# Optimization experiments

Hardware: AMD Instinct MI355X
Metric: run time of the kernel (lower is better)

## Reference

```python
import jax, jax.numpy as jnp
import numpy as np

B, N, E = 2, 16000, 160000
NDIMS, NMEAS, NMODES = 2, 1, 128
IN_DIM, OUT_DIM, FC_DIM = 3, 1, 128
LAYERS = [64, 64, 64, 64]
INV_MIN, INV_MAX = 0.5, 2.0


def setup_inputs() -> dict:
    key = jax.random.key(0)
    ks = jax.random.split(key, 16)
    L = len(LAYERS) - 1
    C = LAYERS[0]
    scale = 1.0 / (C * C)
    u = lambda k, sh, s: jax.random.uniform(k, sh, jnp.float32, -s, s)
    inp = {}
    inp["x"] = jax.random.normal(ks[0], (B, N, IN_DIM), jnp.float32)
    inp["node_mask"] = jnp.ones((B, N, 1), jnp.int32)
    inp["nodes"] = jax.random.uniform(ks[1], (B, N, NDIMS), jnp.float32)
    inp["node_weights"] = jax.random.uniform(ks[2], (B, N, NMEAS), jnp.float32) / N
    inp["directed_edges"] = jax.random.randint(ks[3], (B, E, 2), 0, N, jnp.int32)
    inp["edge_gradient_weights"] = jax.random.normal(ks[4], (B, E, NDIMS), jnp.float32)
    inp["modes"] = jax.random.normal(ks[5], (NMODES, NDIMS, NMEAS), jnp.float32)
    # scaled_logit(1.0, 0.5, 2.0) = log(0.5/1.0)
    inp["inv_L_scale_latent"] = jnp.full((NDIMS, NMEAS), np.log((1.0 - INV_MIN) / (INV_MAX - 1.0)), jnp.float32)
    inp["fc0_W"] = u(ks[6], (C, IN_DIM), 1.0 / np.sqrt(IN_DIM))
    inp["fc0_b"] = jnp.zeros((C,), jnp.float32)
    inp["weights_c"] = u(ks[7], (L, C, C, NMODES, NMEAS), scale)
    inp["weights_s"] = u(ks[8], (L, C, C, NMODES, NMEAS), scale)
    inp["weights_0"] = u(ks[9], (L, C, C, 1, NMEAS), scale)
    inp["ws_W"] = u(ks[10], (L, C, C), 1.0 / np.sqrt(C))
    inp["ws_b"] = jnp.zeros((L, C), jnp.float32)
    inp["gws_W"] = u(ks[11], (L, C, C * NDIMS), 1.0 / np.sqrt(C * NDIMS))
    inp["gws_b"] = jnp.zeros((L, C), jnp.float32)
    inp["fc1_W"] = u(ks[12], (FC_DIM, C), 1.0 / np.sqrt(C))
    inp["fc1_b"] = jnp.zeros((FC_DIM,), jnp.float32)
    inp["fc2_W"] = u(ks[13], (OUT_DIM, FC_DIM), 1.0 / np.sqrt(FC_DIM))
    inp["fc2_b"] = jnp.zeros((OUT_DIM,), jnp.float32)
    return inp


def _forward(x, nodes, node_weights, edge_gradient_weights, modes, inv_L_scale_latent,
             fc0_W, fc0_b, weights_c, weights_s, weights_0, ws_W, ws_b, gws_W, gws_b,
             fc1_W, fc1_b, fc2_W, fc2_b, directed_edges):
    L = weights_c.shape[0]
    n = x.shape[1]
    # scaled sigmoid of latent inverse length scale
    inv_L = INV_MIN + (INV_MAX - INV_MIN) * jax.nn.sigmoid(inv_L_scale_latent)
    smodes = modes * inv_L  # [K, D, W]
    # Fourier bases over all nodes
    temp = jnp.einsum('bxd,kdw->bxkw', nodes, smodes)  # [B, N, K, W]
    bases_c, bases_s = jnp.cos(temp), jnp.sin(temp)
    bases_0 = jnp.ones(temp.shape[:2] + (1, temp.shape[-1]), temp.dtype)
    wnw = node_weights[:, :, None, :]  # [B, N, 1, W]
    wbases_c, wbases_s, wbases_0 = bases_c * wnw, bases_s * wnw, bases_0 * wnw

    tgt = directed_edges[..., 0]  # [B, E]
    src = directed_edges[..., 1]

    def grad_field(f):  # f: [B, C, N] -> [B, C*D, N]
        ft = jnp.transpose(f, (0, 2, 1))  # [B, N, C]
        f_src = jnp.take_along_axis(ft, src[..., None], axis=1)  # [B, E, C]
        f_tgt = jnp.take_along_axis(ft, tgt[..., None], axis=1)
        diff = f_src - f_tgt
        msg = jnp.einsum('bed,bec->becd', edge_gradient_weights, diff)  # [B, E, C, D]
        msg = msg.reshape(msg.shape[0], msg.shape[1], -1)  # [B, E, C*D]
        seg = jax.vmap(lambda m, t: jax.ops.segment_sum(m, t, num_segments=n))(msg, tgt)
        return jnp.transpose(seg, (0, 2, 1))  # [B, C*D, N]

    # lift: fc0 acts on channel dim
    h = jnp.einsum('oi,bni->bon', fc0_W, x) + fc0_b[None, :, None]  # [B, C, N]

    for i in range(L):
        # spectral conv with explicit bases
        x_c = jnp.einsum('bix,bxkw->bikw', h, wbases_c)
        x_s = -jnp.einsum('bix,bxkw->bikw', h, wbases_s)
        x_0 = jnp.einsum('bix,bxkw->bikw', h, wbases_0)
        f_c = jnp.einsum('bikw,iokw->bokw', x_c, weights_c[i]) - jnp.einsum('bikw,iokw->bokw', x_s, weights_s[i])
        f_s = jnp.einsum('bikw,iokw->bokw', x_s, weights_c[i]) + jnp.einsum('bikw,iokw->bokw', x_c, weights_s[i])
        f_0 = jnp.einsum('bikw,iokw->bokw', x_0, weights_0[i])
        x1 = (jnp.einsum('bokw,bxkw->box', f_0, bases_0)
              + 2 * jnp.einsum('bokw,bxkw->box', f_c, bases_c)
              - 2 * jnp.einsum('bokw,bxkw->box', f_s, bases_s))
        # pointwise linear W
        x2 = jnp.einsum('oi,bin->bon', ws_W[i], h) + ws_b[i][None, :, None]
        # differential operator D: gradient then linear
        x3 = jnp.einsum('oi,bin->bon', gws_W[i], grad_field(h)) + gws_b[i][None, :, None]
        h = x1 + x2 + x3
        if i < L - 1:
            h = jax.nn.gelu(h)

    out = jnp.transpose(h, (0, 2, 1))  # [B, N, C]
    out = jax.nn.gelu(jnp.einsum('oc,bnc->bno', fc1_W, out) + fc1_b)
    out = jnp.einsum('oc,bnc->bno', fc2_W, out) + fc2_b
    return out  # [B, N, out_dim]


def reference(x, node_mask, nodes, node_weights, directed_edges, edge_gradient_weights,
              modes, inv_L_scale_latent, fc0_W, fc0_b, weights_c, weights_s, weights_0,
              ws_W, ws_b, gws_W, gws_b, fc1_W, fc1_b, fc2_W, fc2_b):
    del node_mask  # padding mask; all-ones here, not used in the core math
    return _forward(x, nodes, node_weights, edge_gradient_weights, modes, inv_L_scale_latent,
                    fc0_W, fc0_b, weights_c, weights_s, weights_0, ws_W, ws_b, gws_W, gws_b,
                    fc1_W, fc1_b, fc2_W, fc2_b, directed_edges)
```

## Files before the change

### kernel.cpp

```cpp
#include <hip/hip_runtime.h>
#include <math.h>

#define BB 2
#define NN 16000
#define EE 160000
#define KK 128
#define CC 64
#define LL 3
#define RDIM 448
#define S1 125
#define XR 128

__device__ __forceinline__ float gelu_f(float x){
    float x3 = x * x * x;
    return 0.5f * x * (1.f + tanhf(0.7978845608028654f * (x + 0.044715f * x3)));
}

__device__ __forceinline__ void gl2lds16(const float* g, float* l){
    __builtin_amdgcn_global_load_lds(
        (const __attribute__((address_space(1))) void*)g,
        (__attribute__((address_space(3))) void*)l, 16, 0, 0);
}

__global__ __launch_bounds__(256) void k_bases(
    const float* __restrict__ nodes, const float* __restrict__ modes,
    const float* __restrict__ latent, float* __restrict__ cb, float* __restrict__ sb){
    int bid = blockIdx.x;
    int b = bid / 500, x0 = (bid % 500) * 32;
    int t = threadIdx.x;
    __shared__ float sm0[128], sm1[128];
    if (t < 128){
        float i0 = 0.5f + 1.5f / (1.f + expf(-latent[0]));
        float i1 = 0.5f + 1.5f / (1.f + expf(-latent[1]));
        sm0[t] = modes[t*2+0] * i0;
        sm1[t] = modes[t*2+1] * i1;
    }
    __syncthreads();
    int k = t & 127, xh = t >> 7;
    for (int p = 0; p < 16; p++){
        int x = x0 + p*2 + xh;
        size_t nb = (size_t)b*NN + x;
        float n0 = nodes[nb*2], n1 = nodes[nb*2+1];
        float tmp = n0*sm0[k] + n1*sm1[k];
        float sv, cv; sincosf(tmp, &sv, &cv);
        cb[nb*KK + k] = cv;
        sb[nb*KK + k] = sv;
    }
}

__global__ __launch_bounds__(256) void k_fc0(
    const float* __restrict__ x, const float* __restrict__ W,
    const float* __restrict__ bb, float* __restrict__ h0){
    int bid = blockIdx.x;
    int b = bid / 250, x0 = (bid % 250) * 64;
    int t = threadIdx.x, o = t & 63, xg = t >> 6;
    float w0 = W[o*3], w1 = W[o*3+1], w2 = W[o*3+2], bo = bb[o];
    for (int xi = xg; xi < 64; xi += 4){
        size_t xb = (size_t)b*NN + x0 + xi;
        float v0 = x[xb*3], v1 = x[xb*3+1], v2 = x[xb*3+2];
        h0[xb*CC + o] = w0*v0 + w1*v1 + w2*v2 + bo;
    }
}

__global__ __launch_bounds__(256) void csr_hist(
    const int* __restrict__ edges, int* __restrict__ cnt){
    int idx = blockIdx.x * 256 + threadIdx.x;
    if (idx >= BB*EE) return;
    int b = idx / EE;
    int tgt = edges[(size_t)idx*2];
    atomicAdd(&cnt[b*NN + tgt], 1);
}

__global__ __launch_bounds__(1024) void csr_scan(
    const int* __restrict__ cnt, int* __restrict__ rowptr, int* __restrict__ cursor){
    int b = blockIdx.x;
    int t = threadIdx.x;
    __shared__ int lds[1024];
    int base = t * 16;
    int v[16];
    int run = 0;
    #pragma unroll
    for (int j = 0; j < 16; j++){
        int n = base + j;
        int c = (n < NN) ? cnt[b*NN + n] : 0;
        v[j] = run;
        run += c;
    }
    lds[t] = run;
    __syncthreads();
    for (int off = 1; off < 1024; off <<= 1){
        int xv = (t >= off) ? lds[t-off] : 0;
        __syncthreads();
        lds[t] += xv;
        __syncthreads();
    }
    int toff = lds[t] - run;
    #pragma unroll
    for (int j = 0; j < 16; j++){
        int n = base + j;
        if (n < NN){
            int p = toff + v[j];
            rowptr[b*(NN+1) + n] = p;
            cursor[b*NN + n] = p;
        }
    }
    if (t == 1023) rowptr[b*(NN+1) + NN] = lds[1023];
}

__global__ __launch_bounds__(256) void csr_fill(
    const int* __restrict__ edges, const float* __restrict__ egw,
    int* __restrict__ cursor, int* __restrict__ insrc, float2* __restrict__ inw){
    int idx = blockIdx.x * 256 + threadIdx.x;
    if (idx >= BB*EE) return;
    int b = idx / EE;
    int tgt = edges[(size_t)idx*2];
    int src = edges[(size_t)idx*2 + 1];
    int pos = atomicAdd(&cursor[b*NN + tgt], 1);
    insrc[(size_t)b*EE + pos] = src;
    const float2 wv = *(const float2*)&egw[(size_t)idx*2];
    inw[(size_t)b*EE + pos] = wv;
}

struct FwdBuf {
    float hT[16*64];
    float wcT[16*128];
    float wsT[16*128];
    float wv[16];
};

__global__ __launch_bounds__(256) void k1_fwd(
    const float* __restrict__ h, const float* __restrict__ cb,
    const float* __restrict__ sb, const float* __restrict__ nw,
    float* __restrict__ partC, float* __restrict__ partS, float* __restrict__ part0){
    int bid = blockIdx.x;
    int b = bid / S1, s = bid % S1;
    int t = threadIdx.x;
    __shared__ __align__(16) FwdBuf bufs[2];
    int kg = t & 15, ig = t >> 4;
    float accC[4][8] = {};
    float accS[4][8] = {};
    float acc0[4] = {};
    int xbase = s * XR;

    auto STAGE = [&](FwdBuf* d, int ch){
        int xs = xbase + ch*16;
        const float* hb  = &h [((size_t)b*NN + xs)*CC];
        const float* cbb = &cb[((size_t)b*NN + xs)*KK];
        const float* sbb = &sb[((size_t)b*NN + xs)*KK];
        gl2lds16(hb + t*4, &d->hT[(t>>6)*256]);
        #pragma unroll
        for (int rep = 0; rep < 2; rep++){
            int u = rep*256 + t;
            gl2lds16(cbb + u*4, &d->wcT[(u>>6)*256]);
            gl2lds16(sbb + u*4, &d->wsT[(u>>6)*256]);
        }
        if (t < 16) d->wv[t] = nw[b*NN + xs + t];
    };

    STAGE(&bufs[0], 0);
    int cur = 0;
    for (int ch = 0; ch < XR/16; ch++){
        __syncthreads();
        if (ch < XR/16 - 1) STAGE(&bufs[cur^1], ch+1);
        FwdBuf* d = &bufs[cur];
        #pragma unroll
        for (int xx = 0; xx < 16; xx++){
            float wgt = d->wv[xx];
            float4 hv = *(float4*)&d->hT[xx*64 + ig*4];
            float ha0 = hv.x*wgt, ha1 = hv.y*wgt, ha2 = hv.z*wgt, ha3 = hv.w*wgt;
            acc0[0] += ha0; acc0[1] += ha1; acc0[2] += ha2; acc0[3] += ha3;
            #pragma unroll
            for (int j = 0; j < 8; j++){
                int kq = kg + 16*j;
                float cv = d->wcT[xx*128 + kq];
                float sv = d->wsT[xx*128 + kq];
                accC[0][j] += ha0*cv; accC[1][j] += ha1*cv;
                accC[2][j] += ha2*cv; accC[3][j] += ha3*cv;
                accS[0][j] += ha0*sv; accS[1][j] += ha1*sv;
                accS[2][j] += ha2*sv; accS[3][j] += ha3*sv;
            }
        }
        cur ^= 1;
    }
    size_t pbase = (size_t)(b*S1 + s) * CC;
    #pragma unroll
    for (int ii = 0; ii < 4; ii++){
        int i = ig*4 + ii;
        #pragma unroll
        for (int j = 0; j < 8; j++){
            int k = kg + 16*j;
            partC[(pbase + i)*KK + k] = accC[ii][j];
            partS[(pbase + i)*KK + k] = accS[ii][j];
        }
        if (kg == 0) part0[pbase + i] = acc0[ii];
    }
}

__global__ __launch_bounds__(256) void k1_reduce(
    const float* __restrict__ partC, const float* __restrict__ partS,
    float* __restrict__ Sc, float* __restrict__ Ss){
    int b = blockIdx.x >> 6, i = blockIdx.x & 63;
    int t = threadIdx.x;
    int k = t & 127, sh = t >> 7;
    float c0=0,c1=0,c2=0,c3=0, q0=0,q1=0,q2=0,q3=0;
    int s = sh;
    for (; s + 6 < S1; s += 8){
        size_t i0 = ((size_t)(b*S1 + s    )*CC + i)*KK + k;
        size_t i1 = ((size_t)(b*S1 + s + 2)*CC + i)*KK + k;
        size_t i2 = ((size_t)(b*S1 + s + 4)*CC + i)*KK + k;
        size_t i3 = ((size_t)(b*S1 + s + 6)*CC + i)*KK + k;
        c0 += partC[i0]; c1 += partC[i1]; c2 += partC[i2]; c3 += partC[i3];
        q0 += partS[i0]; q1 += partS[i1]; q2 += partS[i2]; q3 += partS[i3];
    }
    for (; s < S1; s += 2){
        size_t i0 = ((size_t)(b*S1 + s)*CC + i)*KK + k;
        c0 += partC[i0]; q0 += partS[i0];
    }
    float sc = (c0+c1)+(c2+c3), ss = (q0+q1)+(q2+q3);
    __shared__ float rC[128], rS[128];
    if (sh){ rC[k] = sc; rS[k] = ss; }
    __syncthreads();
    if (!sh){
        Sc[((size_t)b*CC + i)*KK + k] = sc + rC[k];
        Ss[((size_t)b*CC + i)*KK + k] = ss + rS[k];
    }
}

__global__ __launch_bounds__(256) void k2_mix(
    const float* __restrict__ Sc, const float* __restrict__ Ss,
    const float* __restrict__ part0,
    const float* __restrict__ wc, const float* __restrict__ wsp,
    const float* __restrict__ w0,
    const float* __restrict__ wsb, const float* __restrict__ gwsb,
    const float* __restrict__ wsW, const float* __restrict__ gwsW,
    float* __restrict__ Wbig, float* __restrict__ bias, int l){
    int b = blockIdx.x >> 6, o = blockIdx.x & 63;
    int t = threadIdx.x;
    __shared__ float fc2s[2][128], fs2s[2][128];
    __shared__ float red[64];
    if (t < 64){
        float x0 = 0.f;
        for (int s = 0; s < S1; s++) x0 += part0[(b*S1+s)*CC + t];
        red[t] = x0 * w0[((size_t)l*CC + t)*CC + o];
    }
    int k = t & 127, hf = t >> 7;
    float fc = 0.f, fs = 0.f;
    for (int i = hf*32; i < hf*32 + 32; i++){
        float sc = Sc[(b*CC + i)*KK + k];
        float ss = Ss[(b*CC + i)*KK + k];
        size_t wi = (((size_t)l*CC + i)*CC + o)*KK + k;
        float a = wc[wi], bb2 = wsp[wi];
        fc += sc*a + ss*bb2;
        fs += sc*bb2 - ss*a;
    }
    fc2s[hf][k] = fc; fs2s[hf][k] = fs;
    __syncthreads();
    size_t wb = ((size_t)b*CC + o) * RDIM;
    if (t < 128){
        float FC = fc2s[0][t] + fc2s[1][t];
        float FS = fs2s[0][t] + fs2s[1][t];
        Wbig[wb + t] = 2.f * FC;
        Wbig[wb + 128 + t] = -2.f * FS;
    }
    if (t < 64) Wbig[wb + 256 + t] = wsW[((size_t)l*CC + o)*CC + t];
    if (t >= 64 && t < 192) Wbig[wb + 320 + (t-64)] = gwsW[((size_t)l*CC + o)*128 + (t-64)];
    if (t == 0){
        float f0 = 0.f;
        for (int i = 0; i < 64; i++) f0 += red[i];
        bias[b*CC + o] = f0 + wsb[l*CC + o] + gwsb[l*CC + o];
    }
}

__global__ __launch_bounds__(256) void k_grad(
    const float* __restrict__ h, const int* __restrict__ rowptr,
    const int* __restrict__ insrc, const float2* __restrict__ inw,
    float* __restrict__ seg){
    int bid = blockIdx.x;
    int b = bid / 1000, n0 = (bid % 1000) * 16;
    int w = threadIdx.x >> 6, c = threadIdx.x & 63;
    const float*  hb  = h + (size_t)b*NN*CC;
    const int*    isb = insrc + (size_t)b*EE;
    const float2* iwb = inw + (size_t)b*EE;
    #pragma unroll
    for (int g = 0; g < 4; g++){
        int n = n0 + w*4 + g;
        float hn = hb[(size_t)n*CC + c];
        int p0 = rowptr[b*(NN+1) + n];
        int p1 = rowptr[b*(NN+1) + n + 1];
        float a0 = 0.f, a1 = 0.f;
        int p = p0;
        for (; p + 4 <= p1; p += 4){
            int s0 = isb[p], s1 = isb[p+1], s2 = isb[p+2], s3 = isb[p+3];
            float2 w0 = iwb[p], w1 = iwb[p+1], w2 = iwb[p+2], w3 = iwb[p+3];
            float d0 = hb[(size_t)s0*CC + c] - hn;
            float d1 = hb[(size_t)s1*CC + c] - hn;
            float d2 = hb[(size_t)s2*CC + c] - hn;
            float d3 = hb[(size_t)s3*CC + c] - hn;
            a0 += w0.x*d0 + w1.x*d1 + w2.x*d2 + w3.x*d3;
            a1 += w0.y*d0 + w1.y*d1 + w2.y*d2 + w3.y*d3;
        }
        for (; p < p1; p++){
            int sx = isb[p]; float2 ww = iwb[p];
            float d = hb[(size_t)sx*CC + c] - hn;
            a0 += ww.x*d; a1 += ww.y*d;
        }
        *(float2*)&seg[((size_t)b*NN + n)*128 + 2*c] = make_float2(a0, a1);
    }
}

__global__ __launch_bounds__(256) void k3_gemm(
    const float* __restrict__ Wbig, const float* __restrict__ bias,
    const float* __restrict__ cbase, const float* __restrict__ sbase,
    const float* __restrict__ h, const float* __restrict__ seg,
    float* __restrict__ hout, int applyGelu){
    int bid = blockIdx.x;
    int b = bid / 250, x0 = (bid % 250) * 64;
    int t = threadIdx.x;
    __shared__ __align__(16) float Wl[32][68];
    __shared__ __align__(16) float Vl[32][68];
    int to = t & 15, tx = t >> 4;
    int o0 = to*4, xl = tx*4;
    float acc[4][4] = {};
    for (int ch = 0; ch < 14; ch++){
        const float* src; int kb, rl;
        if (ch < 4){ src = cbase; kb = ch*32; rl = 128; }
        else if (ch < 8){ src = sbase; kb = (ch-4)*32; rl = 128; }
        else if (ch < 10){ src = h; kb = (ch-8)*32; rl = 64; }
        else { src = seg; kb = (ch-10)*32; rl = 128; }
        #pragma unroll
        for (int rep = 0; rep < 2; rep++){
            int u = rep*256 + t;
            int xx = u >> 3, kq = u & 7;
            float4 v = *(const float4*)&src[((size_t)b*NN + x0 + xx)*rl + kb + kq*4];
            Vl[kq*4+0][xx] = v.x; Vl[kq*4+1][xx] = v.y;
            Vl[kq*4+2][xx] = v.z; Vl[kq*4+3][xx] = v.w;
        }
        #pragma unroll
        for (int rep = 0; rep < 2; rep++){
            int u = rep*256 + t;
            int oo = u >> 3, kq = u & 7;
            float4 v = *(const float4*)&Wbig[((size_t)b*CC + oo)*RDIM + ch*32 + kq*4];
            Wl[kq*4+0][oo] = v.x; Wl[kq*4+1][oo] = v.y;
            Wl[kq*4+2][oo] = v.z; Wl[kq*4+3][oo] = v.w;
        }
        __syncthreads();
        #pragma unroll
        for (int kk = 0; kk < 32; kk++){
            float4 wvec = *(float4*)&Wl[kk][o0];
            float4 vvec = *(float4*)&Vl[kk][xl];
            float wa[4] = {wvec.x, wvec.y, wvec.z, wvec.w};
            float va[4] = {vvec.x, vvec.y, vvec.z, vvec.w};
            #pragma unroll
            for (int j = 0; j < 4; j++)
                #pragma unroll
                for (int i = 0; i < 4; i++)
                    acc[j][i] += va[j] * wa[i];
        }
        __syncthreads();
    }
    float bs[4];
    #pragma unroll
    for (int i = 0; i < 4; i++) bs[i] = bias[b*CC + o0 + i];
    #pragma unroll
    for (int j = 0; j < 4; j++){
        float4 r;
        r.x = acc[j][0] + bs[0];
        r.y = acc[j][1] + bs[1];
        r.z = acc[j][2] + bs[2];
        r.w = acc[j][3] + bs[3];
        if (applyGelu){
            r.x = gelu_f(r.x); r.y = gelu_f(r.y);
            r.z = gelu_f(r.z); r.w = gelu_f(r.w);
        }
        *(float4*)&hout[((size_t)b*NN + x0 + xl + j)*CC + o0] = r;
    }
}

__global__ __launch_bounds__(256) void k_head(
    const float* __restrict__ h, const float* __restrict__ W1,
    const float* __restrict__ b1, const float* __restrict__ W2,
    const float* __restrict__ b2, float* __restrict__ out){
    int bid = blockIdx.x;
    int b = bid / 250, n0 = (bid % 250) * 64;
    int t = threadIdx.x, w = t >> 6, f = t & 63;
    __shared__ float Wl[128][65];
    #pragma unroll
    for (int r = 0; r < 8; r++){
        int u = r*256 + t;
        int ff = u >> 4, cq = u & 15;
        float4 v = *(const float4*)&W1[ff*64 + cq*4];
        Wl[ff][cq*4+0] = v.x; Wl[ff][cq*4+1] = v.y;
        Wl[ff][cq*4+2] = v.z; Wl[ff][cq*4+3] = v.w;
    }
    __syncthreads();
    float w2a = W2[f], w2b = W2[64+f];
    float b1a = b1[f], b1b = b1[64+f];
    float b2v = b2[0];
    for (int g = 0; g < 16; g++){
        int n = n0 + w*16 + g;
        float hv = h[((size_t)b*NN + n)*CC + f];
        float a1 = b1a, a2 = b1b;
        #pragma unroll
        for (int c2 = 0; c2 < 64; c2++){
            float xv = __shfl(hv, c2, 64);
            a1 += Wl[f][c2] * xv;
            a2 += Wl[64+f][c2] * xv;
        }
        float p = gelu_f(a1)*w2a + gelu_f(a2)*w2b;
        for (int off = 32; off; off >>= 1) p += __shfl_down(p, off, 64);
        if (f == 0) out[(size_t)b*NN + n] = p + b2v;
    }
}

extern "C" void kernel_launch(void* const* d_in, const int* in_sizes, int n_in,
                              void* d_out, int out_size, void* d_ws, size_t ws_size,
                              hipStream_t stream){
    const float* x_in  = (const float*)d_in[0];
    const float* nodes = (const float*)d_in[2];
    const float* nw    = (const float*)d_in[3];
    const int*   edges = (const int*)d_in[4];
    const float* egw   = (const float*)d_in[5];
    const float* modes = (const float*)d_in[6];
    const float* latent= (const float*)d_in[7];
    const float* fc0W  = (const float*)d_in[8];
    const float* fc0b  = (const float*)d_in[9];
    const float* wc    = (const float*)d_in[10];
    const float* wsp   = (const float*)d_in[11];
    const float* w0    = (const float*)d_in[12];
    const float* wsW   = (const float*)d_in[13];
    const float* wsb   = (const float*)d_in[14];
    const float* gwsW  = (const float*)d_in[15];
    const float* gwsb  = (const float*)d_in[16];
    const float* fc1W  = (const float*)d_in[17];
    const float* fc1b  = (const float*)d_in[18];
    const float* fc2W  = (const float*)d_in[19];
    const float* fc2b  = (const float*)d_in[20];
    float* out = (float*)d_out;

    char* wsbase = (char*)d_ws;
    size_t off = 0;
    auto alloc = [&](size_t bytes) -> void* {
        void* p = wsbase + off;
        off += (bytes + 255) & ~(size_t)255;
        return p;
    };
    float* cb    = (float*)alloc((size_t)BB*NN*KK*4);
    float* sb    = (float*)alloc((size_t)BB*NN*KK*4);
    float* h0    = (float*)alloc((size_t)BB*NN*CC*4);
    float* h1    = (float*)alloc((size_t)BB*NN*CC*4);
    float* seg   = (float*)alloc((size_t)BB*NN*2*CC*4);
    float* partC = (float*)alloc((size_t)BB*S1*CC*KK*4);
    float* partS = (float*)alloc((size_t)BB*S1*CC*KK*4);
    float* part0 = (float*)alloc((size_t)BB*S1*CC*4);
    float* Sc    = (float*)alloc((size_t)BB*CC*KK*4);
    float* Ss    = (float*)alloc((size_t)BB*CC*KK*4);
    float* Wbig  = (float*)alloc((size_t)BB*CC*RDIM*4);
    float* bias  = (float*)alloc((size_t)BB*CC*4);
    int*   cnt   = (int*)alloc((size_t)BB*NN*4);
    int*   rowptr= (int*)alloc((size_t)BB*(NN+4)*4);
    int*   cursor= (int*)alloc((size_t)BB*NN*4);
    int*   insrc = (int*)alloc((size_t)BB*EE*4);
    float2* inw  = (float2*)alloc((size_t)BB*EE*8);

    k_bases<<<BB*500, 256, 0, stream>>>(nodes, modes, latent, cb, sb);
    k_fc0<<<BB*250, 256, 0, stream>>>(x_in, fc0W, fc0b, h0);

    hipMemsetAsync(cnt, 0, (size_t)BB*NN*4, stream);
    csr_hist<<<(BB*EE+255)/256, 256, 0, stream>>>(edges, cnt);
    csr_scan<<<BB, 1024, 0, stream>>>(cnt, rowptr, cursor);
    csr_fill<<<(BB*EE+255)/256, 256, 0, stream>>>(edges, egw, cursor, insrc, inw);

    float* hcur = h0;
    float* hnext = h1;
    for (int l = 0; l < LL; l++){
        k1_fwd<<<BB*S1, 256, 0, stream>>>(hcur, cb, sb, nw, partC, partS, part0);
        k1_reduce<<<BB*CC, 256, 0, stream>>>(partC, partS, Sc, Ss);
        k2_mix<<<BB*CC, 256, 0, stream>>>(Sc, Ss, part0, wc, wsp, w0, wsb, gwsb,
                                          wsW, gwsW, Wbig, bias, l);
        k_grad<<<BB*1000, 256, 0, stream>>>(hcur, rowptr, insrc, inw, seg);
        k3_gemm<<<BB*250, 256, 0, stream>>>(Wbig, bias, cb, sb, hcur, seg, hnext,
                                            (l < LL-1) ? 1 : 0);
        float* tmp = hcur; hcur = hnext; hnext = tmp;
    }
    k_head<<<BB*250, 256, 0, stream>>>(hcur, fc1W, fc1b, fc2W, fc2b, out);
    (void)in_sizes; (void)n_in; (void)out_size; (void)ws_size;
}
```

Measured before the change: 521.4 us.

## Port spectral and mixing GEMMs to split-bf16 MFMA with precomputed transposed operands

Replaces the FP32 FMA loops in k1_fwd and k3_gemm with bf16 MFMA 16x16x32 instructions. Each FP32 operand is split into high and low bf16 parts and three products are accumulated to stay close to FP32 accuracy. The bases kernel, fc0 and the GEMM epilogue now also emit transposed, node-weighted hi/lo copies, and fc0 and k3 produce part0 directly, with reduce and grad kernels reshaped to match. The aim is to trade scalar FMA throughput for matrix-core throughput, at the cost of extra memory traffic for the duplicated bf16 buffers and a small precision risk.

```diff
diff --git a/kernel.cpp b/kernel.cpp
--- a/kernel.cpp
+++ b/kernel.cpp
@@ -7,59 +7,208 @@
 #define KK 128
 #define CC 64
 #define LL 3
-#define RDIM 448
-#define S1 125
-#define XR 128
+
+typedef __attribute__((ext_vector_type(8))) short bf16x8;
+typedef __attribute__((ext_vector_type(4))) float f32x4;
 
 __device__ __forceinline__ float gelu_f(float x){
     float x3 = x * x * x;
     return 0.5f * x * (1.f + tanhf(0.7978845608028654f * (x + 0.044715f * x3)));
 }
-
-__device__ __forceinline__ void gl2lds16(const float* g, float* l){
-    __builtin_amdgcn_global_load_lds(
-        (const __attribute__((address_space(1))) void*)g,
-        (__attribute__((address_space(3))) void*)l, 16, 0, 0);
-}
+__device__ __forceinline__ ushort f2bf(float f){
+    uint u = __float_as_uint(f);
+    u += 0x7fff + ((u >> 16) & 1);
+    return (ushort)(u >> 16);
+}
+__device__ __forceinline__ float bf2f(ushort h){ return __uint_as_float(((uint)h) << 16); }
+__device__ __forceinline__ void fsplit(float v, ushort &hi, ushort &lo){
+    hi = f2bf(v);
+    lo = f2bf(v - bf2f(hi));
+}
+__device__ __forceinline__ uint pk2(ushort a, ushort b){ return (uint)a | ((uint)b << 16); }
 
 __global__ __launch_bounds__(256) void k_bases(
     const float* __restrict__ nodes, const float* __restrict__ modes,
-    const float* __restrict__ latent, float* __restrict__ cb, float* __restrict__ sb){
+    const float* __restrict__ latent, const float* __restrict__ nw,
+    ushort* __restrict__ cbh, ushort* __restrict__ cbl,
+    ushort* __restrict__ sbh, ushort* __restrict__ sbl,
+    ushort* __restrict__ wTh, ushort* __restrict__ wTl){
     int bid = blockIdx.x;
-    int b = bid / 500, x0 = (bid % 500) * 32;
+    int b = bid / 250, x0 = (bid % 250) * 64;
     int t = threadIdx.x;
-    __shared__ float sm0[128], sm1[128];
+    __shared__ float sm0[128], sm1[128], nwv[64];
+    __shared__ uint tc[64][65], ts[64][65];
     if (t < 128){
         float i0 = 0.5f + 1.5f / (1.f + expf(-latent[0]));
         float i1 = 0.5f + 1.5f / (1.f + expf(-latent[1]));
         sm0[t] = modes[t*2+0] * i0;
         sm1[t] = modes[t*2+1] * i1;
     }
-    __syncthreads();
-    int k = t & 127, xh = t >> 7;
-    for (int p = 0; p < 16; p++){
-        int x = x0 + p*2 + xh;
-        size_t nb = (size_t)b*NN + x;
-        float n0 = nodes[nb*2], n1 = nodes[nb*2+1];
-        float tmp = n0*sm0[k] + n1*sm1[k];
-        float sv, cv; sincosf(tmp, &sv, &cv);
-        cb[nb*KK + k] = cv;
-        sb[nb*KK + k] = sv;
+    if (t < 64) nwv[t] = nw[b*NN + x0 + t];
+    __syncthreads();
+    int xloc = t & 63;
+    float n0 = nodes[((size_t)b*NN + x0 + xloc)*2 + 0];
+    float n1 = nodes[((size_t)b*NN + x0 + xloc)*2 + 1];
+    for (int kh = 0; kh < 2; kh++){
+        int kq = t >> 6;
+        #pragma unroll
+        for (int j = 0; j < 16; j++){
+            int kl = kq*16 + j;
+            int k = kh*64 + kl;
+            float tmp = n0*sm0[k] + n1*sm1[k];
+            float sv, cv; sincosf(tmp, &sv, &cv);
+            ushort h_, l_;
+            fsplit(cv, h_, l_); tc[xloc][kl] = pk2(h_, l_);
+            fsplit(sv, h_, l_); ts[xloc][kl] = pk2(h_, l_);
+        }
+        __syncthreads();
+        {
+            int q = t >> 6;
+            size_t base = ((size_t)b*NN + x0 + xloc)*128 + kh*64 + q*16;
+            #pragma unroll
+            for (int g2 = 0; g2 < 2; g2++){
+                uint u0 = tc[xloc][q*16 + g2*8 + 0], u1 = tc[xloc][q*16 + g2*8 + 1];
+                uint u2 = tc[xloc][q*16 + g2*8 + 2], u3 = tc[xloc][q*16 + g2*8 + 3];
+                uint u4 = tc[xloc][q*16 + g2*8 + 4], u5 = tc[xloc][q*16 + g2*8 + 5];
+                uint u6 = tc[xloc][q*16 + g2*8 + 6], u7 = tc[xloc][q*16 + g2*8 + 7];
+                uint4 vh, vl;
+                vh.x = pk2((ushort)u0,(ushort)u1); vh.y = pk2((ushort)u2,(ushort)u3);
+                vh.z = pk2((ushort)u4,(ushort)u5); vh.w = pk2((ushort)u6,(ushort)u7);
+                vl.x = pk2((ushort)(u0>>16),(ushort)(u1>>16)); vl.y = pk2((ushort)(u2>>16),(ushort)(u3>>16));
+                vl.z = pk2((ushort)(u4>>16),(ushort)(u5>>16)); vl.w = pk2((ushort)(u6>>16),(ushort)(u7>>16));
+                *(uint4*)&cbh[base + g2*8] = vh;
+                *(uint4*)&cbl[base + g2*8] = vl;
+                u0 = ts[xloc][q*16 + g2*8 + 0]; u1 = ts[xloc][q*16 + g2*8 + 1];
+                u2 = ts[xloc][q*16 + g2*8 + 2]; u3 = ts[xloc][q*16 + g2*8 + 3];
+                u4 = ts[xloc][q*16 + g2*8 + 4]; u5 = ts[xloc][q*16 + g2*8 + 5];
+                u6 = ts[xloc][q*16 + g2*8 + 6]; u7 = ts[xloc][q*16 + g2*8 + 7];
+                vh.x = pk2((ushort)u0,(ushort)u1); vh.y = pk2((ushort)u2,(ushort)u3);
+                vh.z = pk2((ushort)u4,(ushort)u5); vh.w = pk2((ushort)u6,(ushort)u7);
+                vl.x = pk2((ushort)(u0>>16),(ushort)(u1>>16)); vl.y = pk2((ushort)(u2>>16),(ushort)(u3>>16));
+                vl.z = pk2((ushort)(u4>>16),(ushort)(u5>>16)); vl.w = pk2((ushort)(u6>>16),(ushort)(u7>>16));
+                *(uint4*)&sbh[base + g2*8] = vh;
+                *(uint4*)&sbl[base + g2*8] = vl;
+            }
+        }
+        {
+            int k = t & 63, g = t >> 6;
+            int kgc = kh*64 + k;
+            int kgs = 128 + kh*64 + k;
+            ushort hc[16], lc[16], hs[16], ls[16];
+            #pragma unroll
+            for (int j = 0; j < 16; j++){
+                int xx = g*16 + j;
+                float wgt = nwv[xx];
+                uint uc = tc[xx][k], us = ts[xx][k];
+                float vc = (bf2f((ushort)uc) + bf2f((ushort)(uc>>16))) * wgt;
+                float vs = (bf2f((ushort)us) + bf2f((ushort)(us>>16))) * wgt;
+                fsplit(vc, hc[j], lc[j]);
+                fsplit(vs, hs[j], ls[j]);
+            }
+            size_t wbc = ((size_t)b*256 + kgc)*16000 + x0 + g*16;
+            size_t wbs = ((size_t)b*256 + kgs)*16000 + x0 + g*16;
+            uint4 v;
+            v.x = pk2(hc[0],hc[1]); v.y = pk2(hc[2],hc[3]); v.z = pk2(hc[4],hc[5]); v.w = pk2(hc[6],hc[7]);
+            *(uint4*)&wTh[wbc] = v;
+            v.x = pk2(hc[8],hc[9]); v.y = pk2(hc[10],hc[11]); v.z = pk2(hc[12],hc[13]); v.w = pk2(hc[14],hc[15]);
+            *(uint4*)&wTh[wbc + 8] = v;
+            v.x = pk2(lc[0],lc[1]); v.y = pk2(lc[2],lc[3]); v.z = pk2(lc[4],lc[5]); v.w = pk2(lc[6],lc[7]);
+            *(uint4*)&wTl[wbc] = v;
+            v.x = pk2(lc[8],lc[9]); v.y = pk2(lc[10],lc[11]); v.z = pk2(lc[12],lc[13]); v.w = pk2(lc[14],lc[15]);
+            *(uint4*)&wTl[wbc + 8] = v;
+            v.x = pk2(hs[0],hs[1]); v.y = pk2(hs[2],hs[3]); v.z = pk2(hs[4],hs[5]); v.w = pk2(hs[6],hs[7]);
+            *(uint4*)&wTh[wbs] = v;
+            v.x = pk2(hs[8],hs[9]); v.y = pk2(hs[10],hs[11]); v.z = pk2(hs[12],hs[13]); v.w = pk2(hs[14],hs[15]);
+            *(uint4*)&wTh[wbs + 8] = v;
+            v.x = pk2(ls[0],ls[1]); v.y = pk2(ls[2],ls[3]); v.z = pk2(ls[4],ls[5]); v.w = pk2(ls[6],ls[7]);
+            *(uint4*)&wTl[wbs] = v;
+            v.x = pk2(ls[8],ls[9]); v.y = pk2(ls[10],ls[11]); v.z = pk2(ls[12],ls[13]); v.w = pk2(ls[14],ls[15]);
+            *(uint4*)&wTl[wbs + 8] = v;
+        }
+        __syncthreads();
+    }
+}
+
+__device__ __forceinline__ void write_h_outputs(
+    const float* ot, const float* nws, int b, int s, int x0, int t, int doAux,
+    float* __restrict__ hx, ushort* __restrict__ hxh, ushort* __restrict__ hxl,
+    ushort* __restrict__ hwh, ushort* __restrict__ hwl, float* __restrict__ part0){
+    {
+        int xl = t >> 1, half = t & 1;
+        size_t gb = ((size_t)b*NN + x0 + xl)*64 + half*32;
+        const float* row = &ot[xl*68 + half*32];
+        #pragma unroll
+        for (int j = 0; j < 8; j++){
+            float4 v; v.x = row[j*4]; v.y = row[j*4+1]; v.z = row[j*4+2]; v.w = row[j*4+3];
+            *(float4*)&hx[gb + j*4] = v;
+        }
+        if (doAux){
+            #pragma unroll
+            for (int q = 0; q < 4; q++){
+                ushort h_[8], l_[8];
+                #pragma unroll
+                for (int j = 0; j < 8; j++) fsplit(row[q*8 + j], h_[j], l_[j]);
+                uint4 vh, vl;
+                vh.x = pk2(h_[0],h_[1]); vh.y = pk2(h_[2],h_[3]); vh.z = pk2(h_[4],h_[5]); vh.w = pk2(h_[6],h_[7]);
+                vl.x = pk2(l_[0],l_[1]); vl.y = pk2(l_[2],l_[3]); vl.z = pk2(l_[4],l_[5]); vl.w = pk2(l_[6],l_[7]);
+                *(uint4*)&hxh[gb + q*8] = vh;
+                *(uint4*)&hxl[gb + q*8] = vl;
+            }
+        }
+    }
+    if (doAux){
+        int i = t & 63, g = t >> 6;
+        float a = 0.f;
+        #pragma unroll
+        for (int rep = 0; rep < 4; rep++){
+            int xs = g*32 + rep*8;
+            ushort h_[8], l_[8];
+            #pragma unroll
+            for (int j = 0; j < 8; j++){
+                float v = ot[(xs + j)*68 + i] * nws[xs + j];
+                a += v;
+                fsplit(v, h_[j], l_[j]);
+            }
+            uint4 vh, vl;
+            vh.x = pk2(h_[0],h_[1]); vh.y = pk2(h_[2],h_[3]); vh.z = pk2(h_[4],h_[5]); vh.w = pk2(h_[6],h_[7]);
+            vl.x = pk2(l_[0],l_[1]); vl.y = pk2(l_[2],l_[3]); vl.z = pk2(l_[4],l_[5]); vl.w = pk2(l_[6],l_[7]);
+            size_t wb = (size_t)(b*64 + i)*16000 + x0 + xs;
+            *(uint4*)&hwh[wb] = vh;
+            *(uint4*)&hwl[wb] = vl;
+        }
+        part0[((size_t)(b*125 + s)*4 + g)*64 + i] = a;
     }
 }
 
 __global__ __launch_bounds__(256) void k_fc0(
     const float* __restrict__ x, const float* __restrict__ W,
-    const float* __restrict__ bb, float* __restrict__ h0){
+    const float* __restrict__ bb, const float* __restrict__ nw,
+    float* __restrict__ hx, ushort* __restrict__ hxh, ushort* __restrict__ hxl,
+    ushort* __restrict__ hwh, ushort* __restrict__ hwl, float* __restrict__ part0){
     int bid = blockIdx.x;
-    int b = bid / 250, x0 = (bid % 250) * 64;
-    int t = threadIdx.x, o = t & 63, xg = t >> 6;
-    float w0 = W[o*3], w1 = W[o*3+1], w2 = W[o*3+2], bo = bb[o];
-    for (int xi = xg; xi < 64; xi += 4){
-        size_t xb = (size_t)b*NN + x0 + xi;
-        float v0 = x[xb*3], v1 = x[xb*3+1], v2 = x[xb*3+2];
-        h0[xb*CC + o] = w0*v0 + w1*v1 + w2*v2 + bo;
-    }
+    int b = bid / 125, s = bid % 125;
+    int x0 = s * 128;
+    int t = threadIdx.x;
+    __shared__ float ot[128*68];
+    __shared__ float nws[128];
+    __shared__ float Wf[192], bf_[64];
+    if (t < 192) Wf[t] = W[t];
+    if (t < 64) bf_[t] = bb[t];
+    if (t < 128) nws[t] = nw[b*NN + x0 + t];
+    __syncthreads();
+    {
+        int xl = t >> 1, half = t & 1;
+        float v0 = x[((size_t)b*NN + x0 + xl)*3 + 0];
+        float v1 = x[((size_t)b*NN + x0 + xl)*3 + 1];
+        float v2 = x[((size_t)b*NN + x0 + xl)*3 + 2];
+        #pragma unroll
+        for (int j = 0; j < 32; j++){
+            int o = half*32 + j;
+            ot[xl*68 + o] = Wf[o*3]*v0 + Wf[o*3+1]*v1 + Wf[o*3+2]*v2 + bf_[o];
+        }
+    }
+    __syncthreads();
+    write_h_outputs(ot, nws, b, s, x0, t, 1, hx, hxh, hxl, hwh, hwl, part0);
 }
 
 __global__ __launch_bounds__(256) void csr_hist(
@@ -121,108 +270,87 @@
     inw[(size_t)b*EE + pos] = wv;
 }
 
-struct FwdBuf {
-    float hT[16*64];
-    float wcT[16*128];
-    float wsT[16*128];
-    float wv[16];
-};
-
 __global__ __launch_bounds__(256) void k1_fwd(
-    const float* __restrict__ h, const float* __restrict__ cb,
-    const float* __restrict__ sb, const float* __restrict__ nw,
-    float* __restrict__ partC, float* __restrict__ partS, float* __restrict__ part0){
+    const ushort* __restrict__ hwH, const ushort* __restrict__ hwL,
+    const ushort* __restrict__ wTH, const ushort* __restrict__ wTL,
+    float* __restrict__ part){
     int bid = blockIdx.x;
-    int b = bid / S1, s = bid % S1;
-    int t = threadIdx.x;
-    __shared__ __align__(16) FwdBuf bufs[2];
-    int kg = t & 15, ig = t >> 4;
-    float accC[4][8] = {};
-    float accS[4][8] = {};
-    float acc0[4] = {};
-    int xbase = s * XR;
-
-    auto STAGE = [&](FwdBuf* d, int ch){
-        int xs = xbase + ch*16;
-        const float* hb  = &h [((size_t)b*NN + xs)*CC];
-        const float* cbb = &cb[((size_t)b*NN + xs)*KK];
-        const float* sbb = &sb[((size_t)b*NN + xs)*KK];
-        gl2lds16(hb + t*4, &d->hT[(t>>6)*256]);
-        #pragma unroll
-        for (int rep = 0; rep < 2; rep++){
-            int u = rep*256 + t;
-            gl2lds16(cbb + u*4, &d->wcT[(u>>6)*256]);
-            gl2lds16(sbb + u*4, &d->wsT[(u>>6)*256]);
-        }
-        if (t < 16) d->wv[t] = nw[b*NN + xs + t];
-    };
-
-    STAGE(&bufs[0], 0);
-    int cur = 0;
-    for (int ch = 0; ch < XR/16; ch++){
-        __syncthreads();
-        if (ch < XR/16 - 1) STAGE(&bufs[cur^1], ch+1);
-        FwdBuf* d = &bufs[cur];
-        #pragma unroll
-        for (int xx = 0; xx < 16; xx++){
-            float wgt = d->wv[xx];
-            float4 hv = *(float4*)&d->hT[xx*64 + ig*4];
-            float ha0 = hv.x*wgt, ha1 = hv.y*wgt, ha2 = hv.z*wgt, ha3 = hv.w*wgt;
-            acc0[0] += ha0; acc0[1] += ha1; acc0[2] += ha2; acc0[3] += ha3;
+    int b = bid / 250, s = bid % 250;
+    int x0 = s * 64;
+    int t = threadIdx.x, l = t & 63, w = t >> 6;
+    __shared__ __align__(16) ushort Bh[128*64], Bl[128*64];
+    f32x4 acc[16] = {};
+    bf16x8 Ah[2], Al[2];
+    int i = w*16 + (l & 15);
+    #pragma unroll
+    for (int ks = 0; ks < 2; ks++){
+        size_t ab = (size_t)(b*64 + i)*16000 + x0 + ks*32 + ((l >> 4) * 8);
+        Ah[ks] = *reinterpret_cast<const bf16x8*>(&hwH[ab]);
+        Al[ks] = *reinterpret_cast<const bf16x8*>(&hwL[ab]);
+    }
+    for (int p = 0; p < 2; p++){
+        #pragma unroll
+        for (int it = 0; it < 4; it++){
+            int u = it*256 + t;
+            int kloc = u >> 3, q = u & 7;
+            size_t g = ((size_t)(b*256 + p*128 + kloc))*16000 + x0 + q*8;
+            uint4 vh = *(const uint4*)&wTH[g];
+            uint4 vl = *(const uint4*)&wTL[g];
+            int ldsb = kloc*128 + ((q*16) ^ ((kloc & 7) << 4));
+            *(uint4*)&Bh[ldsb >> 1] = vh;
+            *(uint4*)&Bl[ldsb >> 1] = vl;
+        }
+        __syncthreads();
+        #pragma unroll
+        for (int kt = 0; kt < 8; kt++){
+            int kcol = kt*16 + (l & 15);
+            int ai = p*8 + kt;
             #pragma unroll
-            for (int j = 0; j < 8; j++){
-                int kq = kg + 16*j;
-                float cv = d->wcT[xx*128 + kq];
-                float sv = d->wsT[xx*128 + kq];
-                accC[0][j] += ha0*cv; accC[1][j] += ha1*cv;
-                accC[2][j] += ha2*cv; accC[3][j] += ha3*cv;
-                accS[0][j] += ha0*sv; accS[1][j] += ha1*sv;
-                accS[2][j] += ha2*sv; accS[3][j] += ha3*sv;
+            for (int ks = 0; ks < 2; ks++){
+                int boff = kcol*128 + (((ks*64) + ((l >> 4) * 16)) ^ ((kcol & 7) << 4));
+                bf16x8 bh = *reinterpret_cast<const bf16x8*>(&Bh[boff >> 1]);
+                bf16x8 bl = *reinterpret_cast<const bf16x8*>(&Bl[boff >> 1]);
+                acc[ai] = __builtin_amdgcn_mfma_f32_16x16x32_bf16(Ah[ks], bh, acc[ai], 0, 0, 0);
+                acc[ai] = __builtin_amdgcn_mfma_f32_16x16x32_bf16(Ah[ks], bl, acc[ai], 0, 0, 0);
+                acc[ai] = __builtin_amdgcn_mfma_f32_16x16x32_bf16(Al[ks], bh, acc[ai], 0, 0, 0);
             }
         }
-        cur ^= 1;
-    }
-    size_t pbase = (size_t)(b*S1 + s) * CC;
-    #pragma unroll
-    for (int ii = 0; ii < 4; ii++){
-        int i = ig*4 + ii;
-        #pragma unroll
-        for (int j = 0; j < 8; j++){
-            int k = kg + 16*j;
-            partC[(pbase + i)*KK + k] = accC[ii][j];
-            partS[(pbase + i)*KK + k] = accS[ii][j];
-        }
-        if (kg == 0) part0[pbase + i] = acc0[ii];
-    }
-}
-
-__global__ __launch_bounds__(256) void k1_reduce(
-    const float* __restrict__ partC, const float* __restrict__ partS,
-    float* __restrict__ Sc, float* __restrict__ Ss){
+        __syncthreads();
+    }
+    size_t pb = (size_t)(b*250 + s) * 64 * 256;
+    #pragma unroll
+    for (int nt = 0; nt < 16; nt++){
+        #pragma unroll
+        for (int r = 0; r < 4; r++){
+            int irow = w*16 + (l >> 4)*4 + r;
+            part[pb + (size_t)irow*256 + nt*16 + (l & 15)] = acc[nt][r];
+        }
+    }
+}
+
+__global__ __launch_bounds__(512) void k1_reduce(
+    const float* __restrict__ part, float* __restrict__ Sc, float* __restrict__ Ss){
     int b = blockIdx.x >> 6, i = blockIdx.x & 63;
     int t = threadIdx.x;
-    int k = t & 127, sh = t >> 7;
-    float c0=0,c1=0,c2=0,c3=0, q0=0,q1=0,q2=0,q3=0;
-    int s = sh;
-    for (; s + 6 < S1; s += 8){
-        size_t i0 = ((size_t)(b*S1 + s    )*CC + i)*KK + k;
-        size_t i1 = ((size_t)(b*S1 + s + 2)*CC + i)*KK + k;
-        size_t i2 = ((size_t)(b*S1 + s + 4)*CC + i)*KK + k;
-        size_t i3 = ((size_t)(b*S1 + s + 6)*CC + i)*KK + k;
-        c0 += partC[i0]; c1 += partC[i1]; c2 += partC[i2]; c3 += partC[i3];
-        q0 += partS[i0]; q1 += partS[i1]; q2 += partS[i2]; q3 += partS[i3];
-    }
-    for (; s < S1; s += 2){
-        size_t i0 = ((size_t)(b*S1 + s)*CC + i)*KK + k;
-        c0 += partC[i0]; q0 += partS[i0];
-    }
-    float sc = (c0+c1)+(c2+c3), ss = (q0+q1)+(q2+q3);
-    __shared__ float rC[128], rS[128];
-    if (sh){ rC[k] = sc; rS[k] = ss; }
+    int c = t & 255, sh = t >> 8;
+    float a0=0,a1=0,a2=0,a3=0;
+    int j = sh;
+    for (; j + 6 < 250; j += 8){
+        a0 += part[((size_t)(b*250 + j    )*64 + i)*256 + c];
+        a1 += part[((size_t)(b*250 + j + 2)*64 + i)*256 + c];
+        a2 += part[((size_t)(b*250 + j + 4)*64 + i)*256 + c];
+        a3 += part[((size_t)(b*250 + j + 6)*64 + i)*256 + c];
+    }
+    for (; j < 250; j += 2)
+        a0 += part[((size_t)(b*250 + j)*64 + i)*256 + c];
+    float sum = (a0+a1)+(a2+a3);
+    __shared__ float r2[256];
+    if (sh) r2[c] = sum;
     __syncthreads();
     if (!sh){
-        Sc[((size_t)b*CC + i)*KK + k] = sc + rC[k];
-        Ss[((size_t)b*CC + i)*KK + k] = ss + rS[k];
+        sum += r2[c];
+        if (c < 128) Sc[(size_t)(b*64 + i)*128 + c] = sum;
+        else         Ss[(size_t)(b*64 + i)*128 + (c - 128)] = sum;
     }
 }
 
@@ -233,21 +361,22 @@
     const float* __restrict__ w0,
     const float* __restrict__ wsb, const float* __restrict__ gwsb,
     const float* __restrict__ wsW, const float* __restrict__ gwsW,
-    float* __restrict__ Wbig, float* __restrict__ bias, int l){
+    ushort* __restrict__ WbH, ushort* __restrict__ WbL,
+    float* __restrict__ bias, int l){
     int b = blockIdx.x >> 6, o = blockIdx.x & 63;
     int t = threadIdx.x;
     __shared__ float fc2s[2][128], fs2s[2][128];
     __shared__ float red[64];
     if (t < 64){
         float x0 = 0.f;
-        for (int s = 0; s < S1; s++) x0 += part0[(b*S1+s)*CC + t];
+        for (int s2 = 0; s2 < 500; s2++) x0 += part0[(size_t)(b*500 + s2)*64 + t];
         red[t] = x0 * w0[((size_t)l*CC + t)*CC + o];
     }
     int k = t & 127, hf = t >> 7;
     float fc = 0.f, fs = 0.f;
     for (int i = hf*32; i < hf*32 + 32; i++){
-        float sc = Sc[(b*CC + i)*KK + k];
-        float ss = Ss[(b*CC + i)*KK + k];
+        float sc = Sc[(size_t)(b*CC + i)*KK + k];
+        float ss = Ss[(size_t)(b*CC + i)*KK + k];
         size_t wi = (((size_t)l*CC + i)*CC + o)*KK + k;
         float a = wc[wi], bb2 = wsp[wi];
         fc += sc*a + ss*bb2;
@@ -255,15 +384,22 @@
     }
     fc2s[hf][k] = fc; fs2s[hf][k] = fs;
     __syncthreads();
-    size_t wb = ((size_t)b*CC + o) * RDIM;
+    size_t wb = (size_t)(b*CC + o) * 448;
     if (t < 128){
         float FC = fc2s[0][t] + fc2s[1][t];
         float FS = fs2s[0][t] + fs2s[1][t];
-        Wbig[wb + t] = 2.f * FC;
-        Wbig[wb + 128 + t] = -2.f * FS;
-    }
-    if (t < 64) Wbig[wb + 256 + t] = wsW[((size_t)l*CC + o)*CC + t];
-    if (t >= 64 && t < 192) Wbig[wb + 320 + (t-64)] = gwsW[((size_t)l*CC + o)*128 + (t-64)];
+        ushort h_, l_;
+        fsplit(2.f*FC, h_, l_);
+        WbH[wb + t] = h_; WbL[wb + t] = l_;
+        fsplit(-2.f*FS, h_, l_);
+        WbH[wb + 128 + t] = h_; WbL[wb + 128 + t] = l_;
+    }
+    if (t < 192){
+        float v = (t < 64) ? wsW[((size_t)l*CC + o)*CC + t]
+                           : gwsW[((size_t)l*CC + o)*128 + (t - 64)];
+        ushort h_, l_; fsplit(v, h_, l_);
+        WbH[wb + 256 + t] = h_; WbL[wb + 256 + t] = l_;
+    }
     if (t == 0){
         float f0 = 0.f;
         for (int i = 0; i < 64; i++) f0 += red[i];
@@ -274,16 +410,16 @@
 __global__ __launch_bounds__(256) void k_grad(
     const float* __restrict__ h, const int* __restrict__ rowptr,
     const int* __restrict__ insrc, const float2* __restrict__ inw,
-    float* __restrict__ seg){
+    ushort* __restrict__ segh, ushort* __restrict__ segl){
     int bid = blockIdx.x;
-    int b = bid / 1000, n0 = (bid % 1000) * 16;
+    int b = bid / 2000, n0 = (bid % 2000) * 8;
     int w = threadIdx.x >> 6, c = threadIdx.x & 63;
     const float*  hb  = h + (size_t)b*NN*CC;
     const int*    isb = insrc + (size_t)b*EE;
     const float2* iwb = inw + (size_t)b*EE;
     #pragma unroll
-    for (int g = 0; g < 4; g++){
-        int n = n0 + w*4 + g;
+    for (int g = 0; g < 2; g++){
+        int n = n0 + w*2 + g;
         float hn = hb[(size_t)n*CC + c];
         int p0 = rowptr[b*(NN+1) + n];
         int p1 = rowptr[b*(NN+1) + n + 1];
@@ -304,76 +440,98 @@
             float d = hb[(size_t)sx*CC + c] - hn;
             a0 += ww.x*d; a1 += ww.y*d;
         }
-        *(float2*)&seg[((size_t)b*NN + n)*128 + 2*c] = make_float2(a0, a1);
+        ushort h0_, l0_, h1_, l1_;
+        fsplit(a0, h0_, l0_);
+        fsplit(a1, h1_, l1_);
+        size_t sb2 = ((size_t)b*NN + n)*128 + 2*c;
+        *(uint*)&segh[sb2] = pk2(h0_, h1_);
+        *(uint*)&segl[sb2] = pk2(l0_, l1_);
     }
 }
 
 __global__ __launch_bounds__(256) void k3_gemm(
-    const float* __restrict__ Wbig, const float* __restrict__ bias,
-    const float* __restrict__ cbase, const float* __restrict__ sbase,
-    const float* __restrict__ h, const float* __restrict__ seg,
-    float* __restrict__ hout, int applyGelu){
+    const ushort* __restrict__ WbH, const ushort* __restrict__ WbL,
+    const float* __restrict__ bias,
+    const ushort* __restrict__ cbh, const ushort* __restrict__ cbl,
+    const ushort* __restrict__ sbh, const ushort* __restrict__ sbl,
+    const ushort* __restrict__ hxh, const ushort* __restrict__ hxl,
+    const ushort* __restrict__ sgh, const ushort* __restrict__ sgl,
+    const float* __restrict__ nw,
+    float* __restrict__ hxO, ushort* __restrict__ hxhO, ushort* __restrict__ hxlO,
+    ushort* __restrict__ hwhO, ushort* __restrict__ hwlO, float* __restrict__ part0,
+    int doAux){
     int bid = blockIdx.x;
-    int b = bid / 250, x0 = (bid % 250) * 64;
-    int t = threadIdx.x;
-    __shared__ __align__(16) float Wl[32][68];
-    __shared__ __align__(16) float Vl[32][68];
-    int to = t & 15, tx = t >> 4;
-    int o0 = to*4, xl = tx*4;
-    float acc[4][4] = {};
-    for (int ch = 0; ch < 14; ch++){
-        const float* src; int kb, rl;
-        if (ch < 4){ src = cbase; kb = ch*32; rl = 128; }
-        else if (ch < 8){ src = sbase; kb = (ch-4)*32; rl = 128; }
-        else if (ch < 10){ src = h; kb = (ch-8)*32; rl = 64; }
-        else { src = seg; kb = (ch-10)*32; rl = 128; }
-        #pragma unroll
-        for (int rep = 0; rep < 2; rep++){
-            int u = rep*256 + t;
-            int xx = u >> 3, kq = u & 7;
-            float4 v = *(const float4*)&src[((size_t)b*NN + x0 + xx)*rl + kb + kq*4];
-            Vl[kq*4+0][xx] = v.x; Vl[kq*4+1][xx] = v.y;
-            Vl[kq*4+2][xx] = v.z; Vl[kq*4+3][xx] = v.w;
-        }
-        #pragma unroll
-        for (int rep = 0; rep < 2; rep++){
-            int u = rep*256 + t;
-            int oo = u >> 3, kq = u & 7;
-            float4 v = *(const float4*)&Wbig[((size_t)b*CC + oo)*RDIM + ch*32 + kq*4];
-            Wl[kq*4+0][oo] = v.x; Wl[kq*4+1][oo] = v.y;
-            Wl[kq*4+2][oo] = v.z; Wl[kq*4+3][oo] = v.w;
-        }
-        __syncthreads();
-        #pragma unroll
-        for (int kk = 0; kk < 32; kk++){
-            float4 wvec = *(float4*)&Wl[kk][o0];
-            float4 vvec = *(float4*)&Vl[kk][xl];
-            float wa[4] = {wvec.x, wvec.y, wvec.z, wvec.w};
-            float va[4] = {vvec.x, vvec.y, vvec.z, vvec.w};
+    int b = bid / 125, s = bid % 125, x0 = s * 128;
+    int t = threadIdx.x, l = t & 63, w = t >> 6;
+    __shared__ __align__(16) char smem[34816];
+    ushort* Vh = (ushort*)smem;
+    ushort* Vl = Vh + 8192;
+    __shared__ float nws[128];
+    if (t < 128) nws[t] = nw[b*NN + x0 + t];
+    f32x4 acc[8] = {};
+    int o = w*16 + (l & 15);
+    for (int cc = 0; cc < 7; cc++){
+        const ushort *srcH, *srcL; int rl, co;
+        switch (cc){
+            case 0:  srcH = cbh; srcL = cbl; rl = 128; co = 0;  break;
+            case 1:  srcH = cbh; srcL = cbl; rl = 128; co = 64; break;
+            case 2:  srcH = sbh; srcL = sbl; rl = 128; co = 0;  break;
+            case 3:  srcH = sbh; srcL = sbl; rl = 128; co = 64; break;
+            case 4:  srcH = hxh; srcL = hxl; rl = 64;  co = 0;  break;
+            case 5:  srcH = sgh; srcL = sgl; rl = 128; co = 0;  break;
+            default: srcH = sgh; srcL = sgl; rl = 128; co = 64; break;
+        }
+        __syncthreads();
+        #pragma unroll
+        for (int it = 0; it < 4; it++){
+            int u = it*256 + t;
+            int xl2 = u >> 3, q = u & 7;
+            size_t g = (size_t)(b*NN + x0 + xl2)*rl + co + q*8;
+            uint4 vh = *(const uint4*)&srcH[g];
+            uint4 vl2 = *(const uint4*)&srcL[g];
+            int ldsb = xl2*128 + ((q*16) ^ ((xl2 & 7) << 4));
+            *(uint4*)&Vh[ldsb >> 1] = vh;
+            *(uint4*)&Vl[ldsb >> 1] = vl2;
+        }
+        __syncthreads();
+        bf16x8 Ah[2], Al[2];
+        #pragma unroll
+        for (int ks = 0; ks < 2; ks++){
+            size_t ab = (size_t)(b*64 + o)*448 + cc*64 + ks*32 + ((l >> 4) * 8);
+            Ah[ks] = *reinterpret_cast<const bf16x8*>(&WbH[ab]);
+            Al[ks] = *reinterpret_cast<const bf16x8*>(&WbL[ab]);
+        }
+        #pragma unroll
+        for (int nt = 0; nt < 8; nt++){
+            int xc = nt*16 + (l & 15);
             #pragma unroll
-            for (int j = 0; j < 4; j++)
-                #pragma unroll
-                for (int i = 0; i < 4; i++)
-                    acc[j][i] += va[j] * wa[i];
-        }
-        __syncthreads();
-    }
-    float bs[4];
-    #pragma unroll
-    for (int i = 0; i < 4; i++) bs[i] = bias[b*CC + o0 + i];
-    #pragma unroll
-    for (int j = 0; j < 4; j++){
-        float4 r;
-        r.x = acc[j][0] + bs[0];
-        r.y = acc[j][1] + bs[1];
-        r.z = acc[j][2] + bs[2];
-        r.w = acc[j][3] + bs[3];
-        if (applyGelu){
-            r.x = gelu_f(r.x); r.y = gelu_f(r.y);
-            r.z = gelu_f(r.z); r.w = gelu_f(r.w);
-        }
-        *(float4*)&hout[((size_t)b*NN + x0 + xl + j)*CC + o0] = r;
-    }
+            for (int ks = 0; ks < 2; ks++){
+                int boff = xc*128 + (((ks*64) + ((l >> 4) * 16)) ^ ((xc & 7) << 4));
+                bf16x8 bh = *reinterpret_cast<const bf16x8*>(&Vh[boff >> 1]);
+                bf16x8 bl = *reinterpret_cast<const bf16x8*>(&Vl[boff >> 1]);
+                acc[nt] = __builtin_amdgcn_mfma_f32_16x16x32_bf16(Ah[ks], bh, acc[nt], 0, 0, 0);
+                acc[nt] = __builtin_amdgcn_mfma_f32_16x16x32_bf16(Ah[ks], bl, acc[nt], 0, 0, 0);
+                acc[nt] = __builtin_amdgcn_mfma_f32_16x16x32_bf16(Al[ks], bh, acc[nt], 0, 0, 0);
+            }
+        }
+    }
+    __syncthreads();
+    float* ot = (float*)smem;
+    float bv[4];
+    #pragma unroll
+    for (int r = 0; r < 4; r++) bv[r] = bias[b*64 + w*16 + (l >> 4)*4 + r];
+    #pragma unroll
+    for (int nt = 0; nt < 8; nt++){
+        int xc = nt*16 + (l & 15);
+        #pragma unroll
+        for (int r = 0; r < 4; r++){
+            float v = acc[nt][r] + bv[r];
+            if (doAux) v = gelu_f(v);
+            ot[xc*68 + (w*16 + (l >> 4)*4 + r)] = v;
+        }
+    }
+    __syncthreads();
+    write_h_outputs(ot, nws, b, s, x0, t, doAux, hxO, hxhO, hxlO, hwhO, hwlO, part0);
 }
 
 __global__ __launch_bounds__(256) void k_head(
@@ -444,44 +602,61 @@
         off += (bytes + 255) & ~(size_t)255;
         return p;
     };
-    float* cb    = (float*)alloc((size_t)BB*NN*KK*4);
-    float* sb    = (float*)alloc((size_t)BB*NN*KK*4);
-    float* h0    = (float*)alloc((size_t)BB*NN*CC*4);
-    float* h1    = (float*)alloc((size_t)BB*NN*CC*4);
-    float* seg   = (float*)alloc((size_t)BB*NN*2*CC*4);
-    float* partC = (float*)alloc((size_t)BB*S1*CC*KK*4);
-    float* partS = (float*)alloc((size_t)BB*S1*CC*KK*4);
-    float* part0 = (float*)alloc((size_t)BB*S1*CC*4);
-    float* Sc    = (float*)alloc((size_t)BB*CC*KK*4);
-    float* Ss    = (float*)alloc((size_t)BB*CC*KK*4);
-    float* Wbig  = (float*)alloc((size_t)BB*CC*RDIM*4);
-    float* bias  = (float*)alloc((size_t)BB*CC*4);
-    int*   cnt   = (int*)alloc((size_t)BB*NN*4);
-    int*   rowptr= (int*)alloc((size_t)BB*(NN+4)*4);
-    int*   cursor= (int*)alloc((size_t)BB*NN*4);
-    int*   insrc = (int*)alloc((size_t)BB*EE*4);
+    ushort* cbh = (ushort*)alloc((size_t)BB*NN*128*2);
+    ushort* cbl = (ushort*)alloc((size_t)BB*NN*128*2);
+    ushort* sbh = (ushort*)alloc((size_t)BB*NN*128*2);
+    ushort* sbl = (ushort*)alloc((size_t)BB*NN*128*2);
+    ushort* wTh = (ushort*)alloc((size_t)BB*256*NN*2);
+    ushort* wTl = (ushort*)alloc((size_t)BB*256*NN*2);
+    float*  hx[2];  ushort* hxh[2]; ushort* hxl[2]; ushort* hwh[2]; ushort* hwl[2];
+    for (int i = 0; i < 2; i++){
+        hx[i]  = (float*) alloc((size_t)BB*NN*64*4);
+        hxh[i] = (ushort*)alloc((size_t)BB*NN*64*2);
+        hxl[i] = (ushort*)alloc((size_t)BB*NN*64*2);
+        hwh[i] = (ushort*)alloc((size_t)BB*64*NN*2);
+        hwl[i] = (ushort*)alloc((size_t)BB*64*NN*2);
+    }
+    ushort* segh = (ushort*)alloc((size_t)BB*NN*128*2);
+    ushort* segl = (ushort*)alloc((size_t)BB*NN*128*2);
+    float*  part = (float*) alloc((size_t)BB*250*64*256*4);
+    float*  part0= (float*) alloc((size_t)BB*125*4*64*4);
+    float*  Sc   = (float*) alloc((size_t)BB*64*128*4);
+    float*  Ss   = (float*) alloc((size_t)BB*64*128*4);
+    ushort* WbH  = (ushort*)alloc((size_t)BB*64*448*2);
+    ushort* WbL  = (ushort*)alloc((size_t)BB*64*448*2);
+    float*  bias = (float*) alloc((size_t)BB*64*4);
+    int*   cnt   = (int*)   alloc((size_t)BB*NN*4);
+    int*   rowptr= (int*)   alloc((size_t)BB*(NN+4)*4);
+    int*   cursor= (int*)   alloc((size_t)BB*NN*4);
+    int*   insrc = (int*)   alloc((size_t)BB*EE*4);
     float2* inw  = (float2*)alloc((size_t)BB*EE*8);
 
-    k_bases<<<BB*500, 256, 0, stream>>>(nodes, modes, latent, cb, sb);
-    k_fc0<<<BB*250, 256, 0, stream>>>(x_in, fc0W, fc0b, h0);
+    k_bases<<<BB*250, 256, 0, stream>>>(nodes, modes, latent, nw,
+                                        cbh, cbl, sbh, sbl, wTh, wTl);
+    k_fc0<<<BB*125, 256, 0, stream>>>(x_in, fc0W, fc0b, nw,
+                                      hx[0], hxh[0], hxl[0], hwh[0], hwl[0], part0);
 
     hipMemsetAsync(cnt, 0, (size_t)BB*NN*4, stream);
     csr_hist<<<(BB*EE+255)/256, 256, 0, stream>>>(edges, cnt);
     csr_scan<<<BB, 1024, 0, stream>>>(cnt, rowptr, cursor);
     csr_fill<<<(BB*EE+255)/256, 256, 0, stream>>>(edges, egw, cursor, insrc, inw);
 
-    float* hcur = h0;
-    float* hnext = h1;
+    int cur = 0;
     for (int l = 0; l < LL; l++){
-        k1_fwd<<<BB*S1, 256, 0, stream>>>(hcur, cb, sb, nw, partC, partS, part0);
-        k1_reduce<<<BB*CC, 256, 0, stream>>>(partC, partS, Sc, Ss);
-        k2_mix<<<BB*CC, 256, 0, stream>>>(Sc, Ss, part0, wc, wsp, w0, wsb, gwsb,
-                                          wsW, gwsW, Wbig, bias, l);
-        k_grad<<<BB*1000, 256, 0, stream>>>(hcur, rowptr, insrc, inw, seg);
-        k3_gemm<<<BB*250, 256, 0, stream>>>(Wbig, bias, cb, sb, hcur, seg, hnext,
-                                            (l < LL-1) ? 1 : 0);
-        float* tmp = hcur; hcur = hnext; hnext = tmp;
-    }
-    k_head<<<BB*250, 256, 0, stream>>>(hcur, fc1W, fc1b, fc2W, fc2b, out);
-    (void)in_sizes; (void)n_in; (void)out_size; (void)ws_size;
-}
+        int nxt = cur ^ 1;
+        int doAux = (l < LL-1) ? 1 : 0;
+        k1_fwd<<<BB*250, 256, 0, stream>>>(hwh[cur], hwl[cur], wTh, wTl, part);
+        k1_reduce<<<BB*64, 512, 0, stream>>>(part, Sc, Ss);
+        k2_mix<<<BB*64, 256, 0, stream>>>(Sc, Ss, part0, wc, wsp, w0, wsb, gwsb,
+                                          wsW, gwsW, WbH, WbL, bias, l);
+        k_grad<<<BB*2000, 256, 0, stream>>>(hx[cur], rowptr, insrc, inw, segh, segl);
+        k3_gemm<<<BB*125, 256, 0, stream>>>(WbH, WbL, bias,
+                                            cbh, cbl, sbh, sbl,
+                                            hxh[cur], hxl[cur], segh, segl, nw,
+                                            hx[nxt], hxh[nxt], hxl[nxt],
+                                            hwh[nxt], hwl[nxt], part0, doAux);
+        cur = nxt;
+    }
+    k_head<<<BB*250, 256, 0, stream>>>(hx[cur], fc1W, fc1b, fc2W, fc2b, out);
+    (void)in_sizes; (void)n_in; (void)out_size; (void)ws_size; (void)segh; (void)segl;
+}
```

Result: faster. 509.2 us (-2.3%).
